# Kernel optimization log

Hardware: AMD Instinct MI355X
Metric: run time of the kernel (lower is better)

## Reference

```python
import jax, jax.numpy as jnp
import numpy as np

B, S, E, H, T, K, F = 2, 2048, 768, 12, 128, 16, 3072
DH = E // H


def _ln(x, s, b, eps=1e-6):
    mu = jnp.mean(x, axis=-1, keepdims=True)
    var = jnp.mean(jnp.square(x - mu), axis=-1, keepdims=True)
    return (x - mu) * jax.lax.rsqrt(var + eps) * s + b


def _forward(h, mask, W_topo, b_topo, W_m1, b_m1, W_m2, b_m2, ln_t_s, ln_t_b,
             W_p1, b_p1, W_p2, b_p2, ln1_s, ln1_b, Wq, Wk, Wv, W_gate, b_gate,
             W_o, b_o, ln2_s, ln2_b, W_f1, b_f1, W_f2, b_f2):
    # ---- TopologicalFeatureExtractor (on pre-LN hidden_states) ----
    topo = h @ W_topo + b_topo                                   # [B,S,T]
    hn = h / (jnp.linalg.norm(h, axis=-1, keepdims=True) + 1e-8)
    dist = 1.0 - jnp.einsum('bsd,btd->bst', hn, hn)              # cosine distance [B,S,S]
    dist = jnp.where(jnp.eye(S, dtype=bool)[None], 1e9, dist)    # mask self
    idx = jnp.argsort(dist, axis=-1)[:, :, :K]                   # k-NN indices [B,S,K]
    nd = jnp.take_along_axis(dist, idx, axis=-1)                 # [B,S,K]
    nf = jax.vmap(lambda t, i: t[i])(topo, idx)                  # gather neighbors [B,S,K,T]
    wts = jax.nn.softmax(-nd, axis=-1)[..., None]
    combined = topo + (nf * wts).sum(axis=2)
    t = jax.nn.relu(combined @ W_m1 + b_m1) @ W_m2 + b_m2
    t = _ln(t, ln_t_s, ln_t_b)
    pf = jax.nn.relu(t @ W_p1 + b_p1) @ W_p2 + b_p2              # persistence features [B,S,T]
    # ---- TopologicalAttention (pre-LN residual block) ----
    x = _ln(h, ln1_s, ln1_b)
    q = (x @ Wq).reshape(B, S, H, DH)
    k = (x @ Wk).reshape(B, S, H, DH)
    v = (x @ Wv).reshape(B, S, H, DH)
    scores = jnp.einsum('bqhd,bkhd->bhqk', q, k) / jnp.sqrt(jnp.asarray(DH, jnp.float32))
    scores = jnp.where(mask[:, None, None, :] == 0, -10000.0, scores)
    probs = jax.nn.softmax(scores, axis=-1)
    ctx = jnp.einsum('bhqk,bkhd->bqhd', probs, v).reshape(B, S, E)
    gate = jax.nn.sigmoid(jnp.concatenate([ctx, pf], axis=-1) @ W_gate + b_gate)
    ctx = gate * ctx + (1.0 - gate) * x                          # x is attention's input (post-LN)
    h = h + (ctx @ W_o + b_o)
    # ---- FFN block ----
    y = _ln(h, ln2_s, ln2_b)
    y = jax.nn.gelu(y @ W_f1 + b_f1, approximate=True)
    return h + (y @ W_f2 + b_f2)


def setup_inputs() -> dict:
    key = jax.random.key(0)
    ks = jax.random.split(key, 16)
    w = lambda k, shp: (0.02 * jax.random.normal(k, shp)).astype(jnp.float32)
    z = lambda shp: jnp.zeros(shp, jnp.float32)
    o = lambda shp: jnp.ones(shp, jnp.float32)
    return {
        'hidden_states': jax.random.normal(ks[0], (B, S, E), jnp.float32),
        'attention_mask': jnp.ones((B, S), jnp.int32),
        'W_topo': w(ks[1], (E, T)), 'b_topo': z((T,)),
        'W_m1': w(ks[2], (T, 2 * T)), 'b_m1': z((2 * T,)),
        'W_m2': w(ks[3], (2 * T, T)), 'b_m2': z((T,)),
        'ln_t_s': o((T,)), 'ln_t_b': z((T,)),
        'W_p1': w(ks[4], (T, T)), 'b_p1': z((T,)),
        'W_p2': w(ks[5], (T, T)), 'b_p2': z((T,)),
        'ln1_s': o((E,)), 'ln1_b': z((E,)),
        'Wq': w(ks[6], (E, E)), 'Wk': w(ks[7], (E, E)), 'Wv': w(ks[8], (E, E)),
        'W_gate': w(ks[9], (E + T, E)), 'b_gate': z((E,)),
        'W_o': w(ks[10], (E, E)), 'b_o': z((E,)),
        'ln2_s': o((E,)), 'ln2_b': z((E,)),
        'W_f1': w(ks[11], (E, F)), 'b_f1': z((F,)),
        'W_f2': w(ks[12], (F, E)), 'b_f2': z((E,)),
    }


def reference(hidden_states, attention_mask, W_topo, b_topo, W_m1, b_m1, W_m2, b_m2,
              ln_t_s, ln_t_b, W_p1, b_p1, W_p2, b_p2, ln1_s, ln1_b, Wq, Wk, Wv,
              W_gate, b_gate, W_o, b_o, ln2_s, ln2_b, W_f1, b_f1, W_f2, b_f2):
    return _forward(hidden_states, attention_mask, W_topo, b_topo, W_m1, b_m1, W_m2, b_m2,
                    ln_t_s, ln_t_b, W_p1, b_p1, W_p2, b_p2, ln1_s, ln1_b, Wq, Wk, Wv,
                    W_gate, b_gate, W_o, b_o, ln2_s, ln2_b, W_f1, b_f1, W_f2, b_f2)
```

## Files before the change

kernel.cpp:

```cpp
#include <hip/hip_runtime.h>
#include <hip/hip_bf16.h>
#include <math.h>

#define BDIM 2
#define SDIM 2048
#define EDIM 768
#define HDIM 12
#define TDIM 128
#define KNN  16
#define FDIM 3072
#define DHD  64
#define BS   (BDIM*SDIM)

typedef __attribute__((ext_vector_type(8))) short short8;
typedef __attribute__((ext_vector_type(4))) float f32x4;

__device__ __forceinline__ short f2bf(float f) {
  unsigned u = __float_as_uint(f);
  u = u + 0x7fff + ((u >> 16) & 1);
  return (short)(u >> 16);
}
__device__ __forceinline__ float bf2f(short s) {
  return __uint_as_float(((unsigned)(unsigned short)s) << 16);
}
__device__ __forceinline__ void cp16(void* lds, const void* g) {
  __builtin_amdgcn_global_load_lds(
      (const __attribute__((address_space(1))) unsigned int*)g,
      (__attribute__((address_space(3))) unsigned int*)lds, 16, 0, 0);
}

__device__ __forceinline__ void block_reduce_sum2(float& a, float& b) {
  __shared__ float sa[4], sb[4];
  #pragma unroll
  for (int off = 32; off > 0; off >>= 1) {
    a += __shfl_xor(a, off);
    b += __shfl_xor(b, off);
  }
  int wid = threadIdx.x >> 6;
  if ((threadIdx.x & 63) == 0) { sa[wid] = a; sb[wid] = b; }
  __syncthreads();
  a = sa[0] + sa[1] + sa[2] + sa[3];
  b = sb[0] + sb[1] + sb[2] + sb[3];
}

__global__ __launch_bounds__(256) void cvt_bf_kernel(
    const float* __restrict__ in, short* __restrict__ outp, int n8) {
  int i = blockIdx.x*256 + threadIdx.x;
  if (i < n8) {
    const float4* p4 = (const float4*)(in + (size_t)i*8);
    float4 a = p4[0], b = p4[1];
    short8 pk;
    pk[0]=f2bf(a.x); pk[1]=f2bf(a.y); pk[2]=f2bf(a.z); pk[3]=f2bf(a.w);
    pk[4]=f2bf(b.x); pk[5]=f2bf(b.y); pk[6]=f2bf(b.z); pk[7]=f2bf(b.w);
    *(short8*)(outp + (size_t)i*8) = pk;
  }
}

__global__ __launch_bounds__(256) void wconv_kernel(
    const float* __restrict__ W, short* __restrict__ Wt, int K, int N) {
  __shared__ float tile[64][65];
  const int n0 = blockIdx.x*64, k0 = blockIdx.y*64;
  const int tid = threadIdx.x;
  for (int i = tid; i < 4096; i += 256) {
    int r = i>>6, c = i&63;
    tile[r][c] = W[(size_t)(k0+r)*N + n0 + c];
  }
  __syncthreads();
  for (int i = tid; i < 4096; i += 256) {
    int r = i>>6, c = i&63;
    Wt[(size_t)(n0+r)*K + k0 + c] = f2bf(tile[c][r]);
  }
}

__global__ __launch_bounds__(256) void norm_ln1_kernel(
    const float* __restrict__ h, const float* __restrict__ s,
    const float* __restrict__ bb, short* __restrict__ hh, short* __restrict__ hl,
    float* __restrict__ x, short* __restrict__ xb) {
  int row = blockIdx.x;
  const float* hr = h + (size_t)row * EDIM;
  float v[3], s1 = 0.f, s2 = 0.f;
  #pragma unroll
  for (int t = 0; t < 3; ++t) {
    v[t] = hr[threadIdx.x + 256*t];
    s1 += v[t]; s2 += v[t]*v[t];
  }
  block_reduce_sum2(s1, s2);
  float mu  = s1 * (1.f/EDIM);
  float var = s2 * (1.f/EDIM) - mu*mu;
  float rs  = rsqrtf(var + 1e-6f);
  float invn = 1.f / (sqrtf(s2) + 1e-8f);
  #pragma unroll
  for (int t = 0; t < 3; ++t) {
    int i = threadIdx.x + 256*t;
    size_t idx = (size_t)row*EDIM + i;
    float hnv = v[t]*invn;
    short hi = f2bf(hnv);
    hh[idx] = hi;
    hl[idx] = f2bf(hnv - bf2f(hi));
    float xv = (v[t]-mu)*rs*s[i] + bb[i];
    x[idx] = xv;
    xb[idx] = f2bf(xv);
  }
}

__global__ __launch_bounds__(256) void ln_bf_kernel(
    const float* __restrict__ in, const float* __restrict__ s,
    const float* __restrict__ bb, short* __restrict__ outb) {
  int row = blockIdx.x;
  const float* r = in + (size_t)row * EDIM;
  float v[3], s1 = 0.f, s2 = 0.f;
  #pragma unroll
  for (int t = 0; t < 3; ++t) {
    v[t] = r[threadIdx.x + 256*t];
    s1 += v[t]; s2 += v[t]*v[t];
  }
  block_reduce_sum2(s1, s2);
  float mu  = s1 * (1.f/EDIM);
  float var = s2 * (1.f/EDIM) - mu*mu;
  float rs  = rsqrtf(var + 1e-6f);
  #pragma unroll
  for (int t = 0; t < 3; ++t) {
    int i = threadIdx.x + 256*t;
    outb[(size_t)row*EDIM + i] = f2bf((v[t]-mu)*rs*s[i] + bb[i]);
  }
}

template<int ACT, int OUTBF>
__global__ __launch_bounds__(256) void gemm_mfma(
    const short* __restrict__ A, const short* __restrict__ Wt,
    const float* __restrict__ bias, const float* res,
    float* Cf, short* Cb, int Cb_ld,
    const float* __restrict__ blc, const float* __restrict__ blx,
    int K, int N) {
  __shared__ __align__(16) short As[128*64];
  __shared__ __align__(16) short Bs[128*64];
  const int bm = blockIdx.y*128, bn = blockIdx.x*128;
  const int tid = threadIdx.x;
  const int w = tid>>6, lane = tid&63, l15 = lane&15, g = lane>>4;
  const int wm = (w>>1)*64, wn = (w&1)*64;
  f32x4 acc[4][4] = {};
  for (int k0 = 0; k0 < K; k0 += 64) {
    #pragma unroll
    for (int it = 0; it < 4; ++it) {
      int p = (it*256 + tid)*16;
      int row = p >> 7;
      int slot = (p >> 4) & 7;
      int ss = slot ^ (row & 7);
      cp16((char*)As + it*4096 + w*1024, A  + (size_t)(bm+row)*K + k0 + ss*8);
      cp16((char*)Bs + it*4096 + w*1024, Wt + (size_t)(bn+row)*K + k0 + ss*8);
    }
    __syncthreads();
    #pragma unroll
    for (int ks = 0; ks < 2; ++ks) {
      short8 af[4], bfv[4];
      #pragma unroll
      for (int mt = 0; mt < 4; ++mt) {
        int r = wm + mt*16 + l15;
        af[mt] = *(const short8*)&As[r*64 + (((ks*4+g) ^ (r&7))*8)];
      }
      #pragma unroll
      for (int nt = 0; nt < 4; ++nt) {
        int r = wn + nt*16 + l15;
        bfv[nt] = *(const short8*)&Bs[r*64 + (((ks*4+g) ^ (r&7))*8)];
      }
      #pragma unroll
      for (int mt = 0; mt < 4; ++mt)
        #pragma unroll
        for (int nt = 0; nt < 4; ++nt)
          acc[mt][nt] = __builtin_amdgcn_mfma_f32_16x16x32_bf16(af[mt], bfv[nt], acc[mt][nt], 0, 0, 0);
    }
    __syncthreads();
  }
  #pragma unroll
  for (int mt = 0; mt < 4; ++mt) {
    #pragma unroll
    for (int nt = 0; nt < 4; ++nt) {
      #pragma unroll
      for (int reg = 0; reg < 4; ++reg) {
        int row = bm + wm + mt*16 + g*4 + reg;
        int col = bn + wn + nt*16 + l15;
        float v = acc[mt][nt][reg];
        if (bias) v += bias[col];
        if (ACT == 2) {
          float xx = v;
          float t2 = 0.7978845608028654f*(xx + 0.044715f*xx*xx*xx);
          v = 0.5f*xx*(1.f + tanhf(t2));
        }
        if (ACT == 3) {
          float gg = 1.f/(1.f + expf(-v));
          size_t ix = (size_t)row*EDIM + col;
          float mv = gg*blc[ix] + (1.f-gg)*blx[ix];
          Cb[(size_t)row*Cb_ld + col] = f2bf(mv);
        } else {
          if (res) v += res[(size_t)row*N + col];
          if (OUTBF) Cb[(size_t)row*Cb_ld + col] = f2bf(v);
          else       Cf[(size_t)row*N + col] = v;
        }
      }
    }
  }
}

__global__ __launch_bounds__(256) void dist_mfma(
    const short* __restrict__ Hh, const short* __restrict__ Hl,
    float* __restrict__ dist) {
  __shared__ __align__(16) short Ah[128*64], Al[128*64];
  __shared__ __align__(16) short Bh[128*64], Bl[128*64];
  const int bm = blockIdx.y*128, bn = blockIdx.x*128;
  const int tid = threadIdx.x;
  const int w = tid>>6, lane = tid&63, l15 = lane&15, g = lane>>4;
  const int wm = (w>>1)*64, wn = (w&1)*64;
  f32x4 acc[4][4] = {};
  for (int k0 = 0; k0 < EDIM; k0 += 64) {
    #pragma unroll
    for (int it = 0; it < 4; ++it) {
      int p = (it*256 + tid)*16;
      int row = p >> 7;
      int slot = (p >> 4) & 7;
      int ss = slot ^ (row & 7);
      size_t ga = (size_t)(bm+row)*EDIM + k0 + ss*8;
      size_t gb = (size_t)(bn+row)*EDIM + k0 + ss*8;
      cp16((char*)Ah + it*4096 + w*1024, Hh + ga);
      cp16((char*)Al + it*4096 + w*1024, Hl + ga);
      cp16((char*)Bh + it*4096 + w*1024, Hh + gb);
      cp16((char*)Bl + it*4096 + w*1024, Hl + gb);
    }
    __syncthreads();
    #pragma unroll
    for (int ks = 0; ks < 2; ++ks) {
      short8 ah[4], al[4], bh[4], bl[4];
      #pragma unroll
      for (int mt = 0; mt < 4; ++mt) {
        int r = wm + mt*16 + l15;
        int o = r*64 + (((ks*4+g) ^ (r&7))*8);
        ah[mt] = *(const short8*)&Ah[o];
        al[mt] = *(const short8*)&Al[o];
      }
      #pragma unroll
      for (int nt = 0; nt < 4; ++nt) {
        int r = wn + nt*16 + l15;
        int o = r*64 + (((ks*4+g) ^ (r&7))*8);
        bh[nt] = *(const short8*)&Bh[o];
        bl[nt] = *(const short8*)&Bl[o];
      }
      #pragma unroll
      for (int mt = 0; mt < 4; ++mt)
        #pragma unroll
        for (int nt = 0; nt < 4; ++nt) {
          acc[mt][nt] = __builtin_amdgcn_mfma_f32_16x16x32_bf16(ah[mt], bh[nt], acc[mt][nt], 0, 0, 0);
          acc[mt][nt] = __builtin_amdgcn_mfma_f32_16x16x32_bf16(ah[mt], bl[nt], acc[mt][nt], 0, 0, 0);
          acc[mt][nt] = __builtin_amdgcn_mfma_f32_16x16x32_bf16(al[mt], bh[nt], acc[mt][nt], 0, 0, 0);
        }
    }
    __syncthreads();
  }
  #pragma unroll
  for (int mt = 0; mt < 4; ++mt) {
    #pragma unroll
    for (int nt = 0; nt < 4; ++nt) {
      #pragma unroll
      for (int reg = 0; reg < 4; ++reg) {
        int row = bm + wm + mt*16 + g*4 + reg;
        int col = bn + wn + nt*16 + l15;
        float v = 1.f - acc[mt][nt][reg];
        if (row == col) v = 1e9f;
        dist[(size_t)row*SDIM + col] = v;
      }
    }
  }
}

__global__ __launch_bounds__(256) void topk_kernel(
    const float* __restrict__ dist, const float* __restrict__ topob,
    float* __restrict__ combb) {
  int s = blockIdx.x;
  __shared__ float vals[SDIM];
  __shared__ float wbv[4];
  __shared__ int   wbi[4];
  __shared__ float nd[KNN];
  __shared__ int   nidx[KNN];
  __shared__ float wts[KNN];
  const int tid = threadIdx.x, lane = tid & 63, wid = tid >> 6;
  const float* drow = dist + (size_t)s*SDIM;
  for (int i = tid; i < SDIM; i += 256) vals[i] = drow[i];
  __syncthreads();
  for (int pass = 0; pass < KNN; ++pass) {
    float best = 3e38f; int bidx = SDIM;
    for (int i = tid; i < SDIM; i += 256) {
      float v = vals[i];
      if (v < best) { best = v; bidx = i; }
    }
    #pragma unroll
    for (int off = 32; off > 0; off >>= 1) {
      float ov = __shfl_xor(best, off);
      int   oi = __shfl_xor(bidx, off);
      if (ov < best || (ov == best && oi < bidx)) { best = ov; bidx = oi; }
    }
    if (lane == 0) { wbv[wid] = best; wbi[wid] = bidx; }
    __syncthreads();
    if (tid == 0) {
      float bv = wbv[0]; int bi = wbi[0];
      #pragma unroll
      for (int q2 = 1; q2 < 4; ++q2)
        if (wbv[q2] < bv || (wbv[q2] == bv && wbi[q2] < bi)) { bv = wbv[q2]; bi = wbi[q2]; }
      nd[pass] = bv; nidx[pass] = bi; vals[bi] = 3e38f;
    }
    __syncthreads();
  }
  if (tid == 0) {
    float m = -nd[0];
    for (int k2 = 1; k2 < KNN; ++k2) m = fmaxf(m, -nd[k2]);
    float ssum = 0.f;
    for (int k2 = 0; k2 < KNN; ++k2) { float e = expf(-nd[k2] - m); wts[k2] = e; ssum += e; }
    float inv = 1.f/ssum;
    for (int k2 = 0; k2 < KNN; ++k2) wts[k2] *= inv;
  }
  __syncthreads();
  if (tid < TDIM) {
    float acc = topob[(size_t)s*TDIM + tid];
    #pragma unroll
    for (int k2 = 0; k2 < KNN; ++k2) acc += wts[k2]*topob[(size_t)nidx[k2]*TDIM + tid];
    combb[(size_t)s*TDIM + tid] = acc;
  }
}

__global__ __launch_bounds__(256) void topo_mlp_kernel(
    const float* __restrict__ comb,
    const float* __restrict__ W1, const float* __restrict__ b1,
    const float* __restrict__ W2, const float* __restrict__ b2,
    const float* __restrict__ lns, const float* __restrict__ lnb,
    const float* __restrict__ Wp1, const float* __restrict__ bp1,
    const float* __restrict__ Wp2, const float* __restrict__ bp2,
    short* __restrict__ cat) {
  int row = blockIdx.x;
  __shared__ float c[TDIM], a1[2*TDIM], t2[TDIM];
  __shared__ float red[8];
  const int tid = threadIdx.x;
  if (tid < TDIM) c[tid] = comb[(size_t)row*TDIM + tid];
  __syncthreads();
  {
    float a = b1[tid];
    for (int i = 0; i < TDIM; ++i) a += c[i]*W1[i*2*TDIM + tid];
    a1[tid] = fmaxf(a, 0.f);
  }
  __syncthreads();
  float tval = 0.f;
  if (tid < TDIM) {
    float a = b2[tid];
    for (int i = 0; i < 2*TDIM; ++i) a += a1[i]*W2[i*TDIM + tid];
    tval = a;
  }
  float s1 = (tid < TDIM) ? tval : 0.f;
  float s2 = (tid < TDIM) ? tval*tval : 0.f;
  #pragma unroll
  for (int off = 32; off > 0; off >>= 1) { s1 += __shfl_xor(s1, off); s2 += __shfl_xor(s2, off); }
  if ((tid & 63) == 0) { red[tid>>6] = s1; red[4 + (tid>>6)] = s2; }
  __syncthreads();
  s1 = red[0]+red[1]+red[2]+red[3];
  s2 = red[4]+red[5]+red[6]+red[7];
  float mu  = s1 * (1.f/TDIM);
  float var = s2 * (1.f/TDIM) - mu*mu;
  float rs  = rsqrtf(var + 1e-6f);
  if (tid < TDIM) t2[tid] = (tval - mu)*rs*lns[tid] + lnb[tid];
  __syncthreads();
  if (tid < TDIM) {
    float a = bp1[tid];
    for (int i = 0; i < TDIM; ++i) a += t2[i]*Wp1[i*TDIM + tid];
    a1[tid] = fmaxf(a, 0.f);
  }
  __syncthreads();
  if (tid < TDIM) {
    float a = bp2[tid];
    for (int i = 0; i < TDIM; ++i) a += a1[i]*Wp2[i*TDIM + tid];
    cat[(size_t)row*896 + 768 + tid] = f2bf(a);
  }
}

__global__ __launch_bounds__(256) void attn_mfma(
    const short* __restrict__ qkv, const int* __restrict__ maskp,
    float* __restrict__ ctx, short* __restrict__ ctxb) {
  __shared__ __align__(16) short Ks[64*64];
  __shared__ __align__(16) short Vt[64*64];
  __shared__ __align__(16) short Ps[4*16*64];
  __shared__ float Ms[64];
  const int qb0 = blockIdx.x*64;
  const int hh = blockIdx.y, b = blockIdx.z;
  const int tid = threadIdx.x;
  const int w = tid>>6, lane = tid&63, l15 = lane&15, g = lane>>4;
  short8 qf[2];
  {
    size_t rbase = (size_t)(b*SDIM + qb0 + w*16 + l15)*2304 + hh*DHD;
    qf[0] = *(const short8*)&qkv[rbase + g*8];
    qf[1] = *(const short8*)&qkv[rbase + 32 + g*8];
  }
  f32x4 acc[4] = {};
  float m4[4] = {-1e30f, -1e30f, -1e30f, -1e30f};
  float l4[4] = {};
  for (int kt = 0; kt < SDIM; kt += 64) {
    #pragma unroll
    for (int t = tid; t < 512; t += 256) {
      int row = t>>3, slot = t&7;
      short8 vv = *(const short8*)&qkv[(size_t)(b*SDIM+kt+row)*2304 + 768 + hh*DHD + slot*8];
      *(short8*)&Ks[row*64 + ((slot ^ (row&7))*8)] = vv;
    }
    #pragma unroll
    for (int t = tid; t < 512; t += 256) {
      int d = t&63, r8 = (t>>6)<<3;
      short8 pk;
      #pragma unroll
      for (int j = 0; j < 8; ++j)
        pk[j] = qkv[(size_t)(b*SDIM+kt+r8+j)*2304 + 1536 + hh*DHD + d];
      *(short8*)&Vt[d*64 + (((r8>>3) ^ (d&7))*8)] = pk;
    }
    if (tid < 64) Ms[tid] = (float)maskp[b*SDIM + kt + tid];
    __syncthreads();
    f32x4 s[4] = {};
    #pragma unroll
    for (int ks = 0; ks < 2; ++ks) {
      #pragma unroll
      for (int t = 0; t < 4; ++t) {
        int r = t*16 + l15;
        short8 kb8 = *(const short8*)&Ks[r*64 + (((ks*4+g) ^ (r&7))*8)];
        s[t] = __builtin_amdgcn_mfma_f32_16x16x32_bf16(qf[ks], kb8, s[t], 0, 0, 0);
      }
    }
    float sc[4][4];
    #pragma unroll
    for (int t = 0; t < 4; ++t) {
      float mk = Ms[t*16 + l15];
      #pragma unroll
      for (int reg = 0; reg < 4; ++reg) {
        float val = s[t][reg]*0.125f;
        if (mk == 0.f) val = -10000.f;
        sc[t][reg] = val;
      }
    }
    #pragma unroll
    for (int reg = 0; reg < 4; ++reg) {
      float rm = fmaxf(fmaxf(sc[0][reg], sc[1][reg]), fmaxf(sc[2][reg], sc[3][reg]));
      #pragma unroll
      for (int off = 1; off < 16; off <<= 1) rm = fmaxf(rm, __shfl_xor(rm, off));
      float mnew = fmaxf(m4[reg], rm);
      float corr = __expf(m4[reg] - mnew);
      int qr = g*4 + reg;
      float rs = 0.f;
      #pragma unroll
      for (int t = 0; t < 4; ++t) {
        float p = __expf(sc[t][reg] - mnew);
        rs += p;
        Ps[w*1024 + qr*64 + ((t*16 + l15) ^ ((qr&7)<<3))] = f2bf(p);
      }
      #pragma unroll
      for (int off = 1; off < 16; off <<= 1) rs += __shfl_xor(rs, off);
      l4[reg] = l4[reg]*corr + rs;
      m4[reg] = mnew;
      #pragma unroll
      for (int dt = 0; dt < 4; ++dt) acc[dt][reg] *= corr;
    }
    #pragma unroll
    for (int ks = 0; ks < 2; ++ks) {
      short8 pa = *(const short8*)&Ps[w*1024 + l15*64 + ((ks*32 + g*8) ^ ((l15&7)<<3))];
      #pragma unroll
      for (int dt = 0; dt < 4; ++dt) {
        int r = dt*16 + l15;
        short8 vb8 = *(const short8*)&Vt[r*64 + (((ks*4+g) ^ (r&7))*8)];
        acc[dt] = __builtin_amdgcn_mfma_f32_16x16x32_bf16(pa, vb8, acc[dt], 0, 0, 0);
      }
    }
    __syncthreads();
  }
  float inv[4];
  #pragma unroll
  for (int reg = 0; reg < 4; ++reg) inv[reg] = 1.f / l4[reg];
  #pragma unroll
  for (int dt = 0; dt < 4; ++dt) {
    #pragma unroll
    for (int reg = 0; reg < 4; ++reg) {
      int row = b*SDIM + qb0 + w*16 + g*4 + reg;
      float v = acc[dt][reg]*inv[reg];
      ctx [(size_t)row*EDIM + hh*DHD + dt*16 + l15] = v;
      ctxb[(size_t)row*896  + hh*DHD + dt*16 + l15] = f2bf(v);
    }
  }
}

extern "C" void kernel_launch(void* const* d_in, const int* in_sizes, int n_in,
                              void* d_out, int out_size, void* d_ws, size_t ws_size,
                              hipStream_t stream) {
  const float* h      = (const float*)d_in[0];
  const int*   mask   = (const int*)  d_in[1];
  const float* W_topo = (const float*)d_in[2];
  const float* b_topo = (const float*)d_in[3];
  const float* W_m1   = (const float*)d_in[4];
  const float* b_m1   = (const float*)d_in[5];
  const float* W_m2   = (const float*)d_in[6];
  const float* b_m2   = (const float*)d_in[7];
  const float* ln_t_s = (const float*)d_in[8];
  const float* ln_t_b = (const float*)d_in[9];
  const float* W_p1   = (const float*)d_in[10];
  const float* b_p1   = (const float*)d_in[11];
  const float* W_p2   = (const float*)d_in[12];
  const float* b_p2   = (const float*)d_in[13];
  const float* ln1_s  = (const float*)d_in[14];
  const float* ln1_b  = (const float*)d_in[15];
  const float* Wq     = (const float*)d_in[16];
  const float* Wk     = (const float*)d_in[17];
  const float* Wv     = (const float*)d_in[18];
  const float* W_gate = (const float*)d_in[19];
  const float* b_gate = (const float*)d_in[20];
  const float* W_o    = (const float*)d_in[21];
  const float* b_o    = (const float*)d_in[22];
  const float* ln2_s  = (const float*)d_in[23];
  const float* ln2_b  = (const float*)d_in[24];
  const float* W_f1   = (const float*)d_in[25];
  const float* b_f1   = (const float*)d_in[26];
  const float* W_f2   = (const float*)d_in[27];
  const float* b_f2   = (const float*)d_in[28];
  float* out = (float*)d_out;

  const size_t R = (size_t)BS*EDIM;
  short* wt_topo = (short*)d_ws;
  short* wt_qkv  = wt_topo + (size_t)128*768;
  short* wt_g    = wt_qkv  + (size_t)2304*768;
  short* wt_o    = wt_g    + (size_t)768*896;
  short* wt_f1   = wt_o    + (size_t)768*768;
  short* wt_f2   = wt_f1   + (size_t)3072*768;
  short* regA    = wt_f2   + (size_t)768*3072;
  short* regBCE  = regA + R;
  short* regD    = regBCE + 3*R;
  short* cat     = regD + R;
  float* xf      = (float*)(cat + (size_t)BS*896);
  float* Ff      = xf + R;

  short* h_bf  = regA;
  short* mixb  = regA;
  short* hn_hi = regBCE;
  short* hn_lo = regBCE + R;
  float* topo  = (float*)(regBCE + 2*R);
  float* comb  = topo + (size_t)BS*TDIM;
  short* qkvb  = regBCE;
  short* x_bf  = regD;
  short* y_bf  = regD;
  float* dbuf  = Ff;
  float* ctxf  = Ff;
  short* ybuf  = (short*)Ff;

  cvt_bf_kernel<<<(BS*EDIM/8 + 255)/256, 256, 0, stream>>>(h, h_bf, BS*EDIM/8);
  wconv_kernel<<<dim3(TDIM/64, EDIM/64), 256, 0, stream>>>(W_topo, wt_topo, EDIM, TDIM);
  wconv_kernel<<<dim3(EDIM/64, EDIM/64), 256, 0, stream>>>(Wq, wt_qkv, EDIM, EDIM);
  wconv_kernel<<<dim3(EDIM/64, EDIM/64), 256, 0, stream>>>(Wk, wt_qkv + (size_t)768*768, EDIM, EDIM);
  wconv_kernel<<<dim3(EDIM/64, EDIM/64), 256, 0, stream>>>(Wv, wt_qkv + (size_t)1536*768, EDIM, EDIM);
  wconv_kernel<<<dim3(EDIM/64, 896/64), 256, 0, stream>>>(W_gate, wt_g, 896, EDIM);
  wconv_kernel<<<dim3(EDIM/64, EDIM/64), 256, 0, stream>>>(W_o, wt_o, EDIM, EDIM);
  wconv_kernel<<<dim3(FDIM/64, EDIM/64), 256, 0, stream>>>(W_f1, wt_f1, EDIM, FDIM);
  wconv_kernel<<<dim3(EDIM/64, FDIM/64), 256, 0, stream>>>(W_f2, wt_f2, FDIM, EDIM);
  norm_ln1_kernel<<<BS, 256, 0, stream>>>(h, ln1_s, ln1_b, hn_hi, hn_lo, xf, x_bf);
  gemm_mfma<0,0><<<dim3(1, BS/128), 256, 0, stream>>>(
      h_bf, wt_topo, b_topo, nullptr, topo, nullptr, 0, nullptr, nullptr, EDIM, TDIM);
  for (int b = 0; b < BDIM; ++b) {
    dist_mfma<<<dim3(SDIM/128, SDIM/128), 256, 0, stream>>>(
        hn_hi + (size_t)b*SDIM*EDIM, hn_lo + (size_t)b*SDIM*EDIM, dbuf);
    topk_kernel<<<SDIM, 256, 0, stream>>>(
        dbuf, topo + (size_t)b*SDIM*TDIM, comb + (size_t)b*SDIM*TDIM);
  }
  topo_mlp_kernel<<<BS, 256, 0, stream>>>(comb, W_m1, b_m1, W_m2, b_m2,
                                          ln_t_s, ln_t_b, W_p1, b_p1, W_p2, b_p2, cat);
  gemm_mfma<0,1><<<dim3(2304/128, BS/128), 256, 0, stream>>>(
      x_bf, wt_qkv, nullptr, nullptr, nullptr, qkvb, 2304, nullptr, nullptr, EDIM, 2304);
  attn_mfma<<<dim3(SDIM/64, HDIM, BDIM), 256, 0, stream>>>(qkvb, mask, ctxf, cat);
  gemm_mfma<3,1><<<dim3(EDIM/128, BS/128), 256, 0, stream>>>(
      cat, wt_g, b_gate, nullptr, nullptr, mixb, EDIM, ctxf, xf, 896, EDIM);
  gemm_mfma<0,0><<<dim3(EDIM/128, BS/128), 256, 0, stream>>>(
      mixb, wt_o, b_o, h, out, nullptr, 0, nullptr, nullptr, EDIM, EDIM);
  ln_bf_kernel<<<BS, 256, 0, stream>>>(out, ln2_s, ln2_b, y_bf);
  gemm_mfma<2,1><<<dim3(FDIM/128, BS/128), 256, 0, stream>>>(
      y_bf, wt_f1, b_f1, nullptr, nullptr, ybuf, FDIM, nullptr, nullptr, EDIM, FDIM);
  gemm_mfma<0,0><<<dim3(EDIM/128, BS/128), 256, 0, stream>>>(
      ybuf, wt_f2, b_f2, out, out, nullptr, 0, nullptr, nullptr, FDIM, EDIM);
}
```

Measured before the change: 774.4 us.

## Pre-transpose V, widen attention key tiles, register-resident top-k selection

Adds a separate kernel that writes V transposed per head, so attention can load K and V tiles with 16-byte async copies (cp16) into swizzled LDS instead of gathering V element by element. The attention key tile grows from 64 to 128, which halves the number of loop iterations and syncs at the cost of more LDS and registers. Top-k now keeps each thread's 8 distance values in registers and rescans only the thread that owned the winner, replacing the full LDS rescan on every pass. The trade-off is an extra kernel launch and a round trip of V through global memory.

```diff
diff --git a/kernel.cpp b/kernel.cpp
--- a/kernel.cpp
+++ b/kernel.cpp
@@ -69,6 +69,28 @@
   for (int i = tid; i < 4096; i += 256) {
     int r = i>>6, c = i&63;
     Wt[(size_t)(n0+r)*K + k0 + c] = f2bf(tile[c][r]);
+  }
+}
+
+__global__ __launch_bounds__(256) void vtrans_kernel(
+    const short* __restrict__ qkv, short* __restrict__ vt) {
+  __shared__ short t[64][72];
+  const int s0 = blockIdx.x*64;
+  const int bh = blockIdx.y;
+  const int b = bh / HDIM, h = bh % HDIM;
+  const int tid = threadIdx.x;
+  for (int i = tid; i < 512; i += 256) {
+    int r = i>>3, c8 = (i&7)<<3;
+    *(short8*)&t[r][c8] =
+        *(const short8*)&qkv[(size_t)(b*SDIM+s0+r)*2304 + 1536 + h*DHD + c8];
+  }
+  __syncthreads();
+  for (int i = tid; i < 512; i += 256) {
+    int d = i>>3, c8 = (i&7)<<3;
+    short8 pk;
+    #pragma unroll
+    for (int j = 0; j < 8; ++j) pk[j] = t[c8+j][d];
+    *(short8*)&vt[(size_t)(bh*DHD+d)*SDIM + s0 + c8] = pk;
   }
 }
 
@@ -274,7 +296,6 @@
     const float* __restrict__ dist, const float* __restrict__ topob,
     float* __restrict__ combb) {
   int s = blockIdx.x;
-  __shared__ float vals[SDIM];
   __shared__ float wbv[4];
   __shared__ int   wbi[4];
   __shared__ float nd[KNN];
@@ -282,28 +303,42 @@
   __shared__ float wts[KNN];
   const int tid = threadIdx.x, lane = tid & 63, wid = tid >> 6;
   const float* drow = dist + (size_t)s*SDIM;
-  for (int i = tid; i < SDIM; i += 256) vals[i] = drow[i];
-  __syncthreads();
+  float lv[8];
+  float best = 3e38f; int bidx = 1<<30;
+  #pragma unroll
+  for (int j = 0; j < 8; ++j) {
+    int i = tid + j*256;
+    float v = drow[i];
+    lv[j] = v;
+    if (v < best) { best = v; bidx = i; }
+  }
   for (int pass = 0; pass < KNN; ++pass) {
-    float best = 3e38f; int bidx = SDIM;
-    for (int i = tid; i < SDIM; i += 256) {
-      float v = vals[i];
-      if (v < best) { best = v; bidx = i; }
-    }
+    float bv = best; int bi = bidx;
     #pragma unroll
     for (int off = 32; off > 0; off >>= 1) {
-      float ov = __shfl_xor(best, off);
-      int   oi = __shfl_xor(bidx, off);
-      if (ov < best || (ov == best && oi < bidx)) { best = ov; bidx = oi; }
-    }
-    if (lane == 0) { wbv[wid] = best; wbi[wid] = bidx; }
+      float ov = __shfl_xor(bv, off);
+      int   oi = __shfl_xor(bi, off);
+      if (ov < bv || (ov == bv && oi < bi)) { bv = ov; bi = oi; }
+    }
+    if (lane == 0) { wbv[wid] = bv; wbi[wid] = bi; }
     __syncthreads();
     if (tid == 0) {
-      float bv = wbv[0]; int bi = wbi[0];
+      float fv = wbv[0]; int fi = wbi[0];
       #pragma unroll
       for (int q2 = 1; q2 < 4; ++q2)
-        if (wbv[q2] < bv || (wbv[q2] == bv && wbi[q2] < bi)) { bv = wbv[q2]; bi = wbi[q2]; }
-      nd[pass] = bv; nidx[pass] = bi; vals[bi] = 3e38f;
+        if (wbv[q2] < fv || (wbv[q2] == fv && wbi[q2] < fi)) { fv = wbv[q2]; fi = wbi[q2]; }
+      nd[pass] = fv; nidx[pass] = fi;
+    }
+    __syncthreads();
+    int wi = nidx[pass];
+    if ((wi & 255) == tid) {
+      int jj = wi >> 8;
+      #pragma unroll
+      for (int j = 0; j < 8; ++j) if (j == jj) lv[j] = 3e38f;
+      best = 3e38f; bidx = 1<<30;
+      #pragma unroll
+      for (int j = 0; j < 8; ++j)
+        if (lv[j] < best) { best = lv[j]; bidx = tid + j*256; }
     }
     __syncthreads();
   }
@@ -377,14 +412,16 @@
 }
 
 __global__ __launch_bounds__(256) void attn_mfma(
-    const short* __restrict__ qkv, const int* __restrict__ maskp,
+    const short* __restrict__ qkv, const short* __restrict__ vtb,
+    const int* __restrict__ maskp,
     float* __restrict__ ctx, short* __restrict__ ctxb) {
-  __shared__ __align__(16) short Ks[64*64];
-  __shared__ __align__(16) short Vt[64*64];
-  __shared__ __align__(16) short Ps[4*16*64];
-  __shared__ float Ms[64];
+  __shared__ __align__(16) short Ks[128*64];
+  __shared__ __align__(16) short Vs[64*128];
+  __shared__ __align__(16) short Ps[4*16*128];
+  __shared__ float Ms[128];
   const int qb0 = blockIdx.x*64;
   const int hh = blockIdx.y, b = blockIdx.z;
+  const int bh = b*HDIM + hh;
   const int tid = threadIdx.x;
   const int w = tid>>6, lane = tid&63, l15 = lane&15, g = lane>>4;
   short8 qf[2];
@@ -396,48 +433,48 @@
   f32x4 acc[4] = {};
   float m4[4] = {-1e30f, -1e30f, -1e30f, -1e30f};
   float l4[4] = {};
-  for (int kt = 0; kt < SDIM; kt += 64) {
-    #pragma unroll
-    for (int t = tid; t < 512; t += 256) {
-      int row = t>>3, slot = t&7;
-      short8 vv = *(const short8*)&qkv[(size_t)(b*SDIM+kt+row)*2304 + 768 + hh*DHD + slot*8];
-      *(short8*)&Ks[row*64 + ((slot ^ (row&7))*8)] = vv;
-    }
-    #pragma unroll
-    for (int t = tid; t < 512; t += 256) {
-      int d = t&63, r8 = (t>>6)<<3;
-      short8 pk;
-      #pragma unroll
-      for (int j = 0; j < 8; ++j)
-        pk[j] = qkv[(size_t)(b*SDIM+kt+r8+j)*2304 + 1536 + hh*DHD + d];
-      *(short8*)&Vt[d*64 + (((r8>>3) ^ (d&7))*8)] = pk;
-    }
-    if (tid < 64) Ms[tid] = (float)maskp[b*SDIM + kt + tid];
-    __syncthreads();
-    f32x4 s[4] = {};
+  for (int kt = 0; kt < SDIM; kt += 128) {
+    #pragma unroll
+    for (int it = 0; it < 4; ++it) {
+      int t = it*256 + tid;
+      int row = t>>3, slot = t&7, ss = slot ^ (row&7);
+      cp16((char*)Ks + it*4096 + w*1024,
+           qkv + (size_t)(b*SDIM+kt+row)*2304 + 768 + hh*DHD + ss*8);
+    }
+    #pragma unroll
+    for (int it = 0; it < 4; ++it) {
+      int t = it*256 + tid;
+      int row = t>>4, slot = t&15, ss = slot ^ (row&15);
+      cp16((char*)Vs + it*4096 + w*1024,
+           vtb + (size_t)(bh*DHD+row)*SDIM + kt + ss*8);
+    }
+    if (tid < 128) Ms[tid] = (float)maskp[b*SDIM + kt + tid];
+    __syncthreads();
+    f32x4 s[8] = {};
     #pragma unroll
     for (int ks = 0; ks < 2; ++ks) {
       #pragma unroll
-      for (int t = 0; t < 4; ++t) {
-        int r = t*16 + l15;
+      for (int ct = 0; ct < 8; ++ct) {
+        int r = ct*16 + l15;
         short8 kb8 = *(const short8*)&Ks[r*64 + (((ks*4+g) ^ (r&7))*8)];
-        s[t] = __builtin_amdgcn_mfma_f32_16x16x32_bf16(qf[ks], kb8, s[t], 0, 0, 0);
-      }
-    }
-    float sc[4][4];
-    #pragma unroll
-    for (int t = 0; t < 4; ++t) {
-      float mk = Ms[t*16 + l15];
+        s[ct] = __builtin_amdgcn_mfma_f32_16x16x32_bf16(qf[ks], kb8, s[ct], 0, 0, 0);
+      }
+    }
+    #pragma unroll
+    for (int ct = 0; ct < 8; ++ct) {
+      float mk = Ms[ct*16 + l15];
       #pragma unroll
       for (int reg = 0; reg < 4; ++reg) {
-        float val = s[t][reg]*0.125f;
+        float val = s[ct][reg]*0.125f;
         if (mk == 0.f) val = -10000.f;
-        sc[t][reg] = val;
+        s[ct][reg] = val;
       }
     }
     #pragma unroll
     for (int reg = 0; reg < 4; ++reg) {
-      float rm = fmaxf(fmaxf(sc[0][reg], sc[1][reg]), fmaxf(sc[2][reg], sc[3][reg]));
+      float rm = -1e30f;
+      #pragma unroll
+      for (int ct = 0; ct < 8; ++ct) rm = fmaxf(rm, s[ct][reg]);
       #pragma unroll
       for (int off = 1; off < 16; off <<= 1) rm = fmaxf(rm, __shfl_xor(rm, off));
       float mnew = fmaxf(m4[reg], rm);
@@ -445,10 +482,11 @@
       int qr = g*4 + reg;
       float rs = 0.f;
       #pragma unroll
-      for (int t = 0; t < 4; ++t) {
-        float p = __expf(sc[t][reg] - mnew);
+      for (int ct = 0; ct < 8; ++ct) {
+        float p = __expf(s[ct][reg] - mnew);
         rs += p;
-        Ps[w*1024 + qr*64 + ((t*16 + l15) ^ ((qr&7)<<3))] = f2bf(p);
+        int col = ct*16 + l15;
+        Ps[w*2048 + qr*128 + (((col>>3) ^ qr)<<3) + (col&7)] = f2bf(p);
       }
       #pragma unroll
       for (int off = 1; off < 16; off <<= 1) rs += __shfl_xor(rs, off);
@@ -458,12 +496,12 @@
       for (int dt = 0; dt < 4; ++dt) acc[dt][reg] *= corr;
     }
     #pragma unroll
-    for (int ks = 0; ks < 2; ++ks) {
-      short8 pa = *(const short8*)&Ps[w*1024 + l15*64 + ((ks*32 + g*8) ^ ((l15&7)<<3))];
+    for (int ks2 = 0; ks2 < 4; ++ks2) {
+      short8 pa = *(const short8*)&Ps[w*2048 + l15*128 + (((ks2*4+g) ^ l15)*8)];
       #pragma unroll
       for (int dt = 0; dt < 4; ++dt) {
         int r = dt*16 + l15;
-        short8 vb8 = *(const short8*)&Vt[r*64 + (((ks*4+g) ^ (r&7))*8)];
+        short8 vb8 = *(const short8*)&Vs[r*128 + (((ks2*4+g) ^ (r&15))*8)];
         acc[dt] = __builtin_amdgcn_mfma_f32_16x16x32_bf16(pa, vb8, acc[dt], 0, 0, 0);
       }
     }
@@ -531,6 +569,7 @@
   short* cat     = regD + R;
   float* xf      = (float*)(cat + (size_t)BS*896);
   float* Ff      = xf + R;
+  short* vtb     = (short*)(Ff + (size_t)SDIM*SDIM);
 
   short* h_bf  = regA;
   short* mixb  = regA;
@@ -567,7 +606,8 @@
                                           ln_t_s, ln_t_b, W_p1, b_p1, W_p2, b_p2, cat);
   gemm_mfma<0,1><<<dim3(2304/128, BS/128), 256, 0, stream>>>(
       x_bf, wt_qkv, nullptr, nullptr, nullptr, qkvb, 2304, nullptr, nullptr, EDIM, 2304);
-  attn_mfma<<<dim3(SDIM/64, HDIM, BDIM), 256, 0, stream>>>(qkvb, mask, ctxf, cat);
+  vtrans_kernel<<<dim3(SDIM/64, BDIM*HDIM), 256, 0, stream>>>(qkvb, vtb);
+  attn_mfma<<<dim3(SDIM/64, HDIM, BDIM), 256, 0, stream>>>(qkvb, vtb, mask, ctxf, cat);
   gemm_mfma<3,1><<<dim3(EDIM/128, BS/128), 256, 0, stream>>>(
       cat, wt_g, b_gate, nullptr, nullptr, mixb, EDIM, ctxf, xf, 896, EDIM);
   gemm_mfma<0,0><<<dim3(EDIM/128, BS/128), 256, 0, stream>>>(
```

Measured after the change: 749.2 us. 3.2% less time.
